# Optimization experiments

Hardware: AMD Instinct MI355X
Metric: run time of the kernel (lower is better)

Reference implementation:

```python
import jax, jax.numpy as jnp
from jax import lax
import numpy as np

B, T, H, K = 32, 512, 2048, 128


def setup_inputs() -> dict:
    key = jax.random.key(0)
    k1, k2, k3, k4, k5, k6, k7 = jax.random.split(key, 7)
    hiddens = jax.random.normal(k1, (B, T, H), dtype=jnp.float32)
    mask = jnp.ones((B, T), dtype=jnp.int32)  # mask[:,0] must be on (torchcrf)
    labels = jax.random.randint(k2, (B, T), 0, K)
    W = jax.random.normal(k3, (H, K), dtype=jnp.float32) * 0.02
    b = jnp.zeros((K,), dtype=jnp.float32)
    # torchcrf inits transitions uniform(-0.1, 0.1)
    start_transitions = jax.random.uniform(k4, (K,), minval=-0.1, maxval=0.1)
    end_transitions = jax.random.uniform(k5, (K,), minval=-0.1, maxval=0.1)
    transitions = jax.random.uniform(k6, (K, K), minval=-0.1, maxval=0.1)
    return {"hiddens": hiddens, "mask": mask, "labels": labels, "W": W, "b": b,
            "start_transitions": start_transitions, "end_transitions": end_transitions,
            "transitions": transitions}


def _crf_log_likelihood(emissions, tags, mask, start_t, end_t, trans):
    # emissions: [B,T,K], tags/mask: [B,T]
    Bn, Tn, Kn = emissions.shape
    maskf = mask.astype(emissions.dtype)
    # ---- numerator: score of the gold path ----
    score = start_t[tags[:, 0]] + emissions[jnp.arange(Bn), 0, tags[:, 0]]
    prev, cur = tags[:, :-1], tags[:, 1:]
    emit_cur = jnp.take_along_axis(emissions[:, 1:], cur[..., None], axis=-1)[..., 0]
    score = score + jnp.sum((trans[prev, cur] + emit_cur) * maskf[:, 1:], axis=1)
    last_idx = mask.sum(axis=1).astype(jnp.int32) - 1
    last_tags = jnp.take_along_axis(tags, last_idx[:, None], axis=1)[:, 0]
    score = score + end_t[last_tags]
    # ---- denominator: log partition via stable logsumexp scan ----
    def step(alpha, inp):
        emit_t, m_t = inp  # [B,K], [B]
        nxt = jax.nn.logsumexp(alpha[:, :, None] + trans[None] + emit_t[:, None, :], axis=1)
        alpha = jnp.where(m_t[:, None] > 0, nxt, alpha)
        return alpha, None
    alpha0 = start_t[None, :] + emissions[:, 0]
    emits = jnp.swapaxes(emissions[:, 1:], 0, 1)  # [T-1,B,K]
    ms = jnp.swapaxes(mask[:, 1:], 0, 1)          # [T-1,B]
    alpha, _ = lax.scan(step, alpha0, (emits, ms))
    logZ = jax.nn.logsumexp(alpha + end_t[None, :], axis=1)
    return score - logZ


def _viterbi_decode(emissions, mask, start_t, end_t, trans):
    Bn, Tn, Kn = emissions.shape
    tag_ids = jnp.arange(Kn, dtype=jnp.int32)
    def step(score, inp):
        emit_t, m_t = inp
        cand = score[:, :, None] + trans[None]          # [B,K,K] prev->cur
        bp = jnp.argmax(cand, axis=1).astype(jnp.int32)  # [B,K]
        best = jnp.max(cand, axis=1) + emit_t
        on = m_t[:, None] > 0
        new_score = jnp.where(on, best, score)
        bp = jnp.where(on, bp, tag_ids[None, :])  # identity for padded steps
        return new_score, bp
    score0 = start_t[None, :] + emissions[:, 0]
    emits = jnp.swapaxes(emissions[:, 1:], 0, 1)
    ms = jnp.swapaxes(mask[:, 1:], 0, 1)
    score, history = lax.scan(step, score0, (emits, ms))  # history: [T-1,B,K]
    last_tag = jnp.argmax(score + end_t[None, :], axis=1).astype(jnp.int32)  # [B]
    def back(tag, bp_t):
        tag = jnp.take_along_axis(bp_t, tag[:, None], axis=1)[:, 0]
        return tag, tag
    _, tags_prev = lax.scan(back, last_tag, history, reverse=True)  # [T-1,B]
    tags = jnp.concatenate([tags_prev, last_tag[None, :]], axis=0)  # [T,B]
    return jnp.swapaxes(tags, 0, 1)  # [B,T]


def reference(hiddens, mask, labels, W, b, start_transitions, end_transitions, transitions):
    logits = jnp.einsum('bth,hk->btk', hiddens, W) + b  # emission projection
    decode = _viterbi_decode(logits, mask, start_transitions, end_transitions, transitions)
    llh = _crf_log_likelihood(logits, labels, mask, start_transitions, end_transitions, transitions)
    loss = -jnp.mean(llh)  # -1 * crf(..., reduction='mean')
    return (decode, loss)
```

## Files before the change

kernel.cpp:

```cpp
#include <hip/hip_runtime.h>
#include <hip/hip_bf16.h>
#include <math.h>

#define BB 32
#define TT 512
#define HH 2048
#define KK 128
#define CH 8
#define NC 32
#define NCV 64

#define WS_LOGITS 0
#define WS_SHIST  8388608u
#define WS_BP     16777216u

__device__ __forceinline__ float quad_add(float x) {
    int a = __builtin_amdgcn_update_dpp(0, __float_as_int(x), 0xB1, 0xF, 0xF, true);
    x += __int_as_float(a);
    int b = __builtin_amdgcn_update_dpp(0, __float_as_int(x), 0x4E, 0xF, 0xF, true);
    x += __int_as_float(b);
    return x;
}
__device__ __forceinline__ float quad_max(float x) {
    int a = __builtin_amdgcn_update_dpp(0, __float_as_int(x), 0xB1, 0xF, 0xF, true);
    x = fmaxf(x, __int_as_float(a));
    int b = __builtin_amdgcn_update_dpp(0, __float_as_int(x), 0x4E, 0xF, 0xF, true);
    x = fmaxf(x, __int_as_float(b));
    return x;
}

__device__ __forceinline__ void step_barrier() {
    __builtin_amdgcn_sched_barrier(0);
    asm volatile("s_waitcnt lgkmcnt(0)" ::: "memory");
    __builtin_amdgcn_sched_barrier(0);
    __builtin_amdgcn_s_barrier();
    __builtin_amdgcn_sched_barrier(0);
}

__global__ __launch_bounds__(512) void gemm_k(const float* __restrict__ hid,
                                              const float* __restrict__ Wm,
                                              const float* __restrict__ bias,
                                              float* __restrict__ logits,
                                              float* __restrict__ loss_slot) {
    __shared__ union {
        struct { float As[4][16][72]; float Bs[4][16][132]; } s;
        float4 red[16][128];
    } sm;
    const int tid = threadIdx.x, bid = blockIdx.x;
    if (bid == 0 && tid == 0) loss_slot[0] = 0.0f;
    const int g = tid >> 7, lt = tid & 127;
    const int rowBase = bid * 64;
    const int rowg = lt >> 4, colg = lt & 15;
    const int arow = lt >> 1, ahq = lt & 1;

    float acc[8][8];
#pragma unroll
    for (int i = 0; i < 8; i++)
#pragma unroll
        for (int j = 0; j < 8; j++) acc[i][j] = 0.0f;

    const float* hA = hid + (size_t)(rowBase + arow) * HH + g * 512 + ahq * 8;

    float4 a0, a1, bv[4];
    {
        const int h0 = g * 512;
        a0 = *(const float4*)(hA);
        a1 = *(const float4*)(hA + 4);
#pragma unroll
        for (int r = 0; r < 4; ++r) {
            int idx = r * 128 + lt;
            bv[r] = *(const float4*)(Wm + (size_t)(h0 + (idx >> 5)) * KK + (idx & 31) * 4);
        }
    }

    for (int it = 0; it < 32; ++it) {
        __syncthreads();
        const int hb = ahq * 8;
        sm.s.As[g][hb + 0][arow] = a0.x;
        sm.s.As[g][hb + 1][arow] = a0.y;
        sm.s.As[g][hb + 2][arow] = a0.z;
        sm.s.As[g][hb + 3][arow] = a0.w;
        sm.s.As[g][hb + 4][arow] = a1.x;
        sm.s.As[g][hb + 5][arow] = a1.y;
        sm.s.As[g][hb + 6][arow] = a1.z;
        sm.s.As[g][hb + 7][arow] = a1.w;
#pragma unroll
        for (int r = 0; r < 4; ++r) {
            int idx = r * 128 + lt;
            *(float4*)&sm.s.Bs[g][idx >> 5][(idx & 31) * 4] = bv[r];
        }
        __syncthreads();
        if (it + 1 < 32) {
            const int h0 = g * 512 + (it + 1) * 16;
            a0 = *(const float4*)(hA + (it + 1) * 16);
            a1 = *(const float4*)(hA + (it + 1) * 16 + 4);
#pragma unroll
            for (int r = 0; r < 4; ++r) {
                int idx = r * 128 + lt;
                bv[r] = *(const float4*)(Wm + (size_t)(h0 + (idx >> 5)) * KK + (idx & 31) * 4);
            }
        }
#pragma unroll
        for (int h = 0; h < 16; ++h) {
            float4 aL = *(const float4*)&sm.s.As[g][h][rowg * 8];
            float4 aH = *(const float4*)&sm.s.As[g][h][rowg * 8 + 4];
            float4 b0 = *(const float4*)&sm.s.Bs[g][h][colg * 4];
            float4 b1 = *(const float4*)&sm.s.Bs[g][h][64 + colg * 4];
            float ar[8] = {aL.x, aL.y, aL.z, aL.w, aH.x, aH.y, aH.z, aH.w};
            float br[8] = {b0.x, b0.y, b0.z, b0.w, b1.x, b1.y, b1.z, b1.w};
#pragma unroll
            for (int i = 0; i < 8; i++)
#pragma unroll
                for (int j = 0; j < 8; j++) acc[i][j] = fmaf(ar[i], br[j], acc[i][j]);
        }
    }
    __syncthreads();
    for (int gp = 1; gp <= 3; ++gp) {
        if (g == gp) {
#pragma unroll
            for (int i = 0; i < 8; ++i) {
                sm.red[i * 2][lt] = make_float4(acc[i][0], acc[i][1], acc[i][2], acc[i][3]);
                sm.red[i * 2 + 1][lt] = make_float4(acc[i][4], acc[i][5], acc[i][6], acc[i][7]);
            }
        }
        __syncthreads();
        if (g == 0) {
#pragma unroll
            for (int i = 0; i < 8; ++i) {
                float4 r0 = sm.red[i * 2][lt];
                float4 r1 = sm.red[i * 2 + 1][lt];
                acc[i][0] += r0.x; acc[i][1] += r0.y; acc[i][2] += r0.z; acc[i][3] += r0.w;
                acc[i][4] += r1.x; acc[i][5] += r1.y; acc[i][6] += r1.z; acc[i][7] += r1.w;
            }
        }
        __syncthreads();
    }
    if (g == 0) {
        float4 bb0 = *(const float4*)(bias + colg * 4);
        float4 bb1 = *(const float4*)(bias + 64 + colg * 4);
#pragma unroll
        for (int i = 0; i < 8; ++i) {
            int row = rowBase + rowg * 8 + i;
            *(float4*)(logits + (size_t)row * KK + colg * 4) =
                make_float4(acc[i][0] + bb0.x, acc[i][1] + bb0.y, acc[i][2] + bb0.z, acc[i][3] + bb0.w);
            *(float4*)(logits + (size_t)row * KK + 64 + colg * 4) =
                make_float4(acc[i][4] + bb1.x, acc[i][5] + bb1.y, acc[i][6] + bb1.z, acc[i][7] + bb1.w);
        }
    }
}

struct SMemB {
    float ubuf[2][144];
    float red[4];
};

__global__ __launch_bounds__(256, 1) void scan_k(const float* __restrict__ logits,
                                                 const int* __restrict__ mask,
                                                 const int* __restrict__ labels,
                                                 const float* __restrict__ startT,
                                                 const float* __restrict__ endT,
                                                 const float* __restrict__ trans,
                                                 float* __restrict__ shist,
                                                 float* __restrict__ out) {
    __shared__ SMemB sm;
    const int tid = threadIdx.x;
    const int bid = blockIdx.x;
    const float L2E = 1.4426950408889634f;
    const int s = tid & 3;
    const int jb = tid >> 2;
    const int j0 = jb * 2;
    const int padw = j0 + 4 * (j0 >> 5);
    const int lane = tid & 63;

    if (bid < BB) {
        const int b = bid;
        const float* lrow = logits + (size_t)b * TT * KK;
        unsigned long long mb[8];
#pragma unroll
        for (int c = 0; c < 8; ++c) mb[c] = __ballot(mask[b * TT + c * 64 + lane] != 0);
        float V0[32], V1[32];
#pragma unroll
        for (int k = 0; k < 32; k++) {
            V0[k] = exp2f(trans[(s * 32 + k) * KK + j0] * L2E);
            V1[k] = exp2f(trans[(s * 32 + k) * KK + j0 + 1] * L2E);
        }
        float a0_ = (startT[j0] + lrow[j0]) * L2E;
        float a1_ = (startT[j0 + 1] + lrow[j0 + 1]) * L2E;
        float OFF = (startT[0] + lrow[0]) * L2E;
        float S0_ = exp2f(a0_ - OFF);
        float S1_ = exp2f(a1_ - OFF);
        if (s == 0) {
            sm.ubuf[0][padw] = S0_;
            sm.ubuf[0][padw + 1] = S1_;
        }
        float2 emc[CH], emn[CH];
#pragma unroll
        for (int d = 0; d < CH; ++d) emc[d] = *(const float2*)(lrow + (size_t)d * KK + j0);
        __syncthreads();
        int cur = 0;
        for (int c = 0; c < NC; ++c) {
#pragma unroll
            for (int r = 0; r < CH; ++r) {
                const int t = c * CH + r;
                if (r == 0 && c + 1 < NC) {
#pragma unroll
                    for (int d = 0; d < CH; ++d)
                        emn[d] = *(const float2*)(lrow + (size_t)((c + 1) * CH + d) * KK + j0);
                }
                if (t > 0 && ((mb[t >> 6] >> (t & 63)) & 1ull)) {
                    const float* ub = &sm.ubuf[cur][s * 36];
                    float u00 = sm.ubuf[cur][0];
                    float uu[32];
#pragma unroll
                    for (int cc = 0; cc < 8; ++cc) {
                        float4 v = *(const float4*)(ub + cc * 4);
                        uu[cc * 4] = v.x; uu[cc * 4 + 1] = v.y; uu[cc * 4 + 2] = v.z; uu[cc * 4 + 3] = v.w;
                    }
                    float2 em = emc[r];
                    float p0e = 0.f, p0o = 0.f, p1e = 0.f, p1o = 0.f;
#pragma unroll
                    for (int k = 0; k < 32; k += 2) {
                        p0e = fmaf(uu[k], V0[k], p0e);
                        p1e = fmaf(uu[k], V1[k], p1e);
                        p0o = fmaf(uu[k + 1], V0[k + 1], p0o);
                        p1o = fmaf(uu[k + 1], V1[k + 1], p1o);
                    }
                    float w0 = quad_add(p0e + p0o);
                    float w1 = quad_add(p1e + p1o);
                    float rinv = __builtin_amdgcn_rcpf(u00);
                    OFF += log2f(u00);
                    S0_ = w0 * (exp2f(em.x * L2E) * rinv);
                    S1_ = w1 * (exp2f(em.y * L2E) * rinv);
                    if (s == 0) {
                        sm.ubuf[cur ^ 1][padw] = S0_;
                        sm.ubuf[cur ^ 1][padw + 1] = S1_;
                    }
                    cur ^= 1;
                }
                step_barrier();
            }
#pragma unroll
            for (int d = 0; d < CH; ++d) emc[d] = emn[d];
        }
        if (s == 0) {
            out[b * TT + j0] = S0_;
            out[b * TT + j0 + 1] = S1_;
        }
        if (tid == 0) out[b * TT + 384] = OFF;

        float part = 0.0f;
        for (int tt = tid; tt < TT; tt += 256) {
            if (tt == 0) {
                int l0 = labels[b * TT];
                part += startT[l0] + lrow[l0];
            } else if (mask[b * TT + tt]) {
                int lc = labels[b * TT + tt];
                int lp = labels[b * TT + tt - 1];
                part += trans[lp * KK + lc] + lrow[(size_t)tt * KK + lc];
            }
        }
#pragma unroll
        for (int d = 1; d < 64; d <<= 1) part += __shfl_xor(part, d, 64);
        int wid = tid >> 6;
        if (lane == 0) sm.red[wid] = part;
        __syncthreads();
        if (tid == 0) {
            int total = 0;
#pragma unroll
            for (int c = 0; c < 8; ++c) total += __popcll(mb[c]);
            float score = sm.red[0] + sm.red[1] + sm.red[2] + sm.red[3];
            score += endT[labels[b * TT + total - 1]];
            out[b * TT + 386] = score;
        }
    } else if (bid < 2 * BB) {
        const int b = bid - BB;
        const float* lrow = logits + (size_t)b * TT * KK;
        unsigned long long mb[4];
#pragma unroll
        for (int c = 0; c < 4; ++c) mb[c] = __ballot(mask[b * TT + 256 + c * 64 + lane] != 0);
        float V0[32], V1[32];
#pragma unroll
        for (int k = 0; k < 32; k++) {
            V0[k] = exp2f(trans[j0 * KK + s * 32 + k] * L2E);
            V1[k] = exp2f(trans[(j0 + 1) * KK + s * 32 + k] * L2E);
        }
        float OFF = endT[0] * L2E;
        float S0_ = exp2f(endT[j0] * L2E - OFF);
        float S1_ = exp2f(endT[j0 + 1] * L2E - OFF);
        {
            float2 e511 = *(const float2*)(lrow + (size_t)511 * KK + j0);
            if (s == 0) {
                sm.ubuf[0][padw] = exp2f(e511.x * L2E) * S0_;
                sm.ubuf[0][padw + 1] = exp2f(e511.y * L2E) * S1_;
            }
        }
        float2 emc[CH], emn[CH];
#pragma unroll
        for (int d = 0; d < CH; ++d) emc[d] = *(const float2*)(lrow + (size_t)(510 - d) * KK + j0);
        __syncthreads();
        int cur = 0;
        for (int c = 0; c < NC; ++c) {
#pragma unroll
            for (int r = 0; r < CH; ++r) {
                const int t = 511 - (c * CH + r);
                if (r == 0 && c + 1 < NC) {
#pragma unroll
                    for (int d = 0; d < CH; ++d)
                        emn[d] = *(const float2*)(lrow + (size_t)(510 - (c + 1) * CH - d) * KK + j0);
                }
                if ((mb[(t - 256) >> 6] >> ((t - 256) & 63)) & 1ull) {
                    const float* ub = &sm.ubuf[cur][s * 36];
                    float u00 = sm.ubuf[cur][0];
                    float uu[32];
#pragma unroll
                    for (int cc = 0; cc < 8; ++cc) {
                        float4 v = *(const float4*)(ub + cc * 4);
                        uu[cc * 4] = v.x; uu[cc * 4 + 1] = v.y; uu[cc * 4 + 2] = v.z; uu[cc * 4 + 3] = v.w;
                    }
                    float p0e = 0.f, p0o = 0.f, p1e = 0.f, p1o = 0.f;
#pragma unroll
                    for (int k = 0; k < 32; k += 2) {
                        p0e = fmaf(uu[k], V0[k], p0e);
                        p1e = fmaf(uu[k], V1[k], p1e);
                        p0o = fmaf(uu[k + 1], V0[k + 1], p0o);
                        p1o = fmaf(uu[k + 1], V1[k + 1], p1o);
                    }
                    float w0 = quad_add(p0e + p0o);
                    float w1 = quad_add(p1e + p1o);
                    float rinv = __builtin_amdgcn_rcpf(u00);
                    OFF += log2f(u00);
                    S0_ = w0 * rinv;
                    S1_ = w1 * rinv;
                }
                float2 em = emc[r];
                if (s == 0) {
                    sm.ubuf[cur ^ 1][padw] = exp2f(em.x * L2E) * S0_;
                    sm.ubuf[cur ^ 1][padw + 1] = exp2f(em.y * L2E) * S1_;
                }
                cur ^= 1;
                step_barrier();
            }
#pragma unroll
            for (int d = 0; d < CH; ++d) emc[d] = emn[d];
        }
        if (s == 0) {
            out[b * TT + 128 + j0] = S0_;
            out[b * TT + 128 + j0 + 1] = S1_;
        }
        if (tid == 0) out[b * TT + 385] = OFF;
    } else {
        const int b = bid - 2 * BB;
        const float* lrow = logits + (size_t)b * TT * KK;
        float* hist = shist + (size_t)b * TT * KK;
        unsigned long long mb[8];
#pragma unroll
        for (int c = 0; c < 8; ++c) mb[c] = __ballot(mask[b * TT + c * 64 + lane] != 0);
        float T0[32], T1[32];
#pragma unroll
        for (int k = 0; k < 32; k++) {
            T0[k] = trans[(s * 32 + k) * KK + j0];
            T1[k] = trans[(s * 32 + k) * KK + j0 + 1];
        }
        float s0_ = startT[j0] + lrow[j0];
        float s1_ = startT[j0 + 1] + lrow[j0 + 1];
        if (s == 0) {
            sm.ubuf[0][padw] = s0_;
            sm.ubuf[0][padw + 1] = s1_;
        } else if (s == 1) {
            *(float2*)(hist + j0) = make_float2(s0_, s1_);
        }
        float2 emc[CH], emn[CH], hb[CH];
#pragma unroll
        for (int d = 0; d < CH; ++d) emc[d] = *(const float2*)(lrow + (size_t)d * KK + j0);
        __syncthreads();
        int cur = 0;
        for (int c = 0; c < NCV; ++c) {
#pragma unroll
            for (int r = 0; r < CH; ++r) {
                const int t = c * CH + r;
                if (r == 0 && c + 1 < NCV) {
#pragma unroll
                    for (int d = 0; d < CH; ++d)
                        emn[d] = *(const float2*)(lrow + (size_t)((c + 1) * CH + d) * KK + j0);
                }
                if (t > 0 && ((mb[t >> 6] >> (t & 63)) & 1ull)) {
                    const float* ub = &sm.ubuf[cur][s * 36];
                    float uu[32];
#pragma unroll
                    for (int cc = 0; cc < 8; ++cc) {
                        float4 v = *(const float4*)(ub + cc * 4);
                        uu[cc * 4] = v.x; uu[cc * 4 + 1] = v.y; uu[cc * 4 + 2] = v.z; uu[cc * 4 + 3] = v.w;
                    }
                    float2 em = emc[r];
                    float m0a = -3.0e38f, m0b = -3.0e38f, m1a = -3.0e38f, m1b = -3.0e38f;
#pragma unroll
                    for (int k = 0; k < 32; k += 4) {
                        m0a = fmaxf(m0a, fmaxf(uu[k] + T0[k], uu[k + 1] + T0[k + 1]));
                        m0b = fmaxf(m0b, fmaxf(uu[k + 2] + T0[k + 2], uu[k + 3] + T0[k + 3]));
                        m1a = fmaxf(m1a, fmaxf(uu[k] + T1[k], uu[k + 1] + T1[k + 1]));
                        m1b = fmaxf(m1b, fmaxf(uu[k + 2] + T1[k + 2], uu[k + 3] + T1[k + 3]));
                    }
                    float m0 = quad_max(fmaxf(m0a, m0b));
                    float m1 = quad_max(fmaxf(m1a, m1b));
                    s0_ = m0 + em.x;
                    s1_ = m1 + em.y;
                    if (s == 0) {
                        sm.ubuf[cur ^ 1][padw] = s0_;
                        sm.ubuf[cur ^ 1][padw + 1] = s1_;
                    }
                    cur ^= 1;
                }
                hb[r] = make_float2(s0_, s1_);
                step_barrier();
            }
            if (s == 1) {
#pragma unroll
                for (int r = 0; r < CH; ++r)
                    *(float2*)(hist + (size_t)(c * CH + r) * KK + j0) = hb[r];
            }
#pragma unroll
            for (int d = 0; d < CH; ++d) emc[d] = emn[d];
        }
    }
}

__global__ __launch_bounds__(256) void bp_k(const float* __restrict__ shist,
                                            const float* __restrict__ trans,
                                            const int* __restrict__ mask,
                                            unsigned char* __restrict__ bp) {
    const int t = blockIdx.x + 1;
    const int tid = threadIdx.x;
    const int j = tid & 127, bg = tid >> 7;
    __shared__ float sc[BB][KK];
#pragma unroll
    for (int r = 0; r < 4; ++r) {
        int f = tid + r * 256;
        int bb2 = f >> 5, c4 = (f & 31) * 4;
        *(float4*)&sc[bb2][c4] = *(const float4*)&shist[(size_t)bb2 * TT * KK + (size_t)(t - 1) * KK + c4];
    }
    __syncthreads();
    float m[16];
    int idx[16];
#pragma unroll
    for (int c = 0; c < 16; c++) { m[c] = -3.0e38f; idx[c] = 0; }
    for (int i4 = 0; i4 < 32; ++i4) {
        const int ib = i4 * 4;
        float tr0 = trans[(ib + 0) * KK + j];
        float tr1 = trans[(ib + 1) * KK + j];
        float tr2 = trans[(ib + 2) * KK + j];
        float tr3 = trans[(ib + 3) * KK + j];
#pragma unroll
        for (int c = 0; c < 16; c++) {
            float4 s4 = *(const float4*)&sc[bg + 2 * c][ib];
            float c0 = s4.x + tr0, c1 = s4.y + tr1, c2 = s4.z + tr2, c3 = s4.w + tr3;
            if (c0 > m[c]) { m[c] = c0; idx[c] = ib; }
            if (c1 > m[c]) { m[c] = c1; idx[c] = ib + 1; }
            if (c2 > m[c]) { m[c] = c2; idx[c] = ib + 2; }
            if (c3 > m[c]) { m[c] = c3; idx[c] = ib + 3; }
        }
    }
#pragma unroll
    for (int c = 0; c < 16; c++) {
        int bb2 = bg + 2 * c;
        int v = idx[c];
        if (mask[bb2 * TT + t] == 0) v = j;
        bp[(size_t)bb2 * TT * KK + (size_t)t * KK + j] = (unsigned char)v;
    }
}

__global__ __launch_bounds__(512) void bt_k(const float* __restrict__ shist,
                                            const float* __restrict__ endT,
                                            const unsigned char* __restrict__ bp,
                                            float* __restrict__ out) {
    const int b = blockIdx.x;
    const int tid = threadIdx.x;
    const int lane = tid & 63, w = tid >> 6;
    __shared__ float cb[128];
    __shared__ float pb[128];
    __shared__ int tagbuf[512];
    __shared__ int handoff;
    if (tid < 128) {
        cb[tid] = shist[(size_t)b * TT * KK + (size_t)(TT - 1) * KK + tid] + endT[tid];
        pb[tid] = out[b * TT + tid] * out[b * TT + 128 + tid];
    }
    float offA = out[b * TT + 384];
    float offB = out[b * TT + 385];
    float score = out[b * TT + 386];
    unsigned int reg[64];
    const unsigned char* bpb = bp + (size_t)b * TT * KK;
#pragma unroll
    for (int r = 0; r < 64; r++) {
        int t_row = w * 64 + 1 + r;
        unsigned int v = 0;
        if (t_row < TT) v = *(const unsigned short*)(bpb + (size_t)t_row * KK + lane * 2);
        reg[r] = v;
    }
    __syncthreads();
    if (tid == 0) {
        float mm = cb[0];
        int bi = 0;
        for (int i = 1; i < 128; i++)
            if (cb[i] > mm) { mm = cb[i]; bi = i; }
        tagbuf[TT - 1] = bi;
        handoff = bi;
        float sum = 0.0f;
        for (int i = 0; i < 128; i++) sum += pb[i];
        float logZ = (offA + offB + log2f(sum)) * 0.6931471805599453f;
        float llh = score - logZ;
        atomicAdd(out + BB * TT, -llh * (1.0f / 32.0f));
    }
    __syncthreads();
    for (int ph = 7; ph >= 0; --ph) {
        if (w == ph) {
            int tag = handoff;
#pragma unroll
            for (int r = 63; r >= 0; --r) {
                int t_row = ph * 64 + 1 + r;
                if (t_row < TT) {
                    unsigned int vv = (unsigned int)__shfl((int)reg[r], tag >> 1, 64);
                    tag = (int)((vv >> ((tag & 1) * 8)) & 0xffu);
                    if (lane == 0) tagbuf[t_row - 1] = tag;
                }
            }
            if (lane == 0) handoff = tag;
        }
        __syncthreads();
    }
    out[b * TT + tid] = (float)tagbuf[tid];
}

extern "C" void kernel_launch(void* const* d_in, const int* in_sizes, int n_in,
                              void* d_out, int out_size, void* d_ws, size_t ws_size,
                              hipStream_t stream) {
    const float* hid = (const float*)d_in[0];
    const int* mask = (const int*)d_in[1];
    const int* labels = (const int*)d_in[2];
    const float* Wm = (const float*)d_in[3];
    const float* bias = (const float*)d_in[4];
    const float* startT = (const float*)d_in[5];
    const float* endT = (const float*)d_in[6];
    const float* trans = (const float*)d_in[7];
    float* out = (float*)d_out;
    char* ws = (char*)d_ws;

    float* logits = (float*)(ws + WS_LOGITS);
    float* shist = (float*)(ws + WS_SHIST);
    unsigned char* bp = (unsigned char*)(ws + WS_BP);

    gemm_k<<<256, 512, 0, stream>>>(hid, Wm, bias, logits, out + BB * TT);
    scan_k<<<96, 256, 0, stream>>>(logits, mask, labels, startT, endT, trans, shist, out);
    bp_k<<<TT - 1, 256, 0, stream>>>(shist, trans, mask, bp);
    bt_k<<<BB, 512, 0, stream>>>(shist, endT, bp, out);
}
```

Measured before the change: 623.6 us.

## Merge forward/backward CRF scans and Viterbi pairs into 512-thread blocks

The forward and backward partition-function scans for one batch now run as two 256-thread halves of a single 512-thread block, each with its own shared buffer. Viterbi scans are likewise packed two batches per block, halving the grid from 96 to 48 blocks. The intent is to use fewer CUs and cut launch and scheduling overhead. The cost is that every per-step barrier now synchronises 8 waves instead of 4, which could lengthen the serial critical path.

```diff
diff --git a/kernel.cpp b/kernel.cpp
--- a/kernel.cpp
+++ b/kernel.cpp
@@ -150,11 +150,11 @@
 }
 
 struct SMemB {
-    float ubuf[2][144];
-    float red[4];
+    float ubuf[2][2][144];
+    float red[8];
 };
 
-__global__ __launch_bounds__(256, 1) void scan_k(const float* __restrict__ logits,
+__global__ __launch_bounds__(512, 1) void scan_k(const float* __restrict__ logits,
                                                  const int* __restrict__ mask,
                                                  const int* __restrict__ labels,
                                                  const float* __restrict__ startT,
@@ -166,190 +166,197 @@
     const int tid = threadIdx.x;
     const int bid = blockIdx.x;
     const float L2E = 1.4426950408889634f;
-    const int s = tid & 3;
-    const int jb = tid >> 2;
+    const int half = tid >> 8;
+    const int htid = tid & 255;
+    const int s = htid & 3;
+    const int jb = htid >> 2;
     const int j0 = jb * 2;
     const int padw = j0 + 4 * (j0 >> 5);
-    const int lane = tid & 63;
+    const int lane = htid & 63;
+    float (*ub2)[144] = sm.ubuf[half];
 
     if (bid < BB) {
         const int b = bid;
         const float* lrow = logits + (size_t)b * TT * KK;
-        unsigned long long mb[8];
-#pragma unroll
-        for (int c = 0; c < 8; ++c) mb[c] = __ballot(mask[b * TT + c * 64 + lane] != 0);
-        float V0[32], V1[32];
-#pragma unroll
-        for (int k = 0; k < 32; k++) {
-            V0[k] = exp2f(trans[(s * 32 + k) * KK + j0] * L2E);
-            V1[k] = exp2f(trans[(s * 32 + k) * KK + j0 + 1] * L2E);
-        }
-        float a0_ = (startT[j0] + lrow[j0]) * L2E;
-        float a1_ = (startT[j0 + 1] + lrow[j0 + 1]) * L2E;
-        float OFF = (startT[0] + lrow[0]) * L2E;
-        float S0_ = exp2f(a0_ - OFF);
-        float S1_ = exp2f(a1_ - OFF);
-        if (s == 0) {
-            sm.ubuf[0][padw] = S0_;
-            sm.ubuf[0][padw + 1] = S1_;
-        }
-        float2 emc[CH], emn[CH];
-#pragma unroll
-        for (int d = 0; d < CH; ++d) emc[d] = *(const float2*)(lrow + (size_t)d * KK + j0);
-        __syncthreads();
-        int cur = 0;
-        for (int c = 0; c < NC; ++c) {
-#pragma unroll
-            for (int r = 0; r < CH; ++r) {
-                const int t = c * CH + r;
-                if (r == 0 && c + 1 < NC) {
-#pragma unroll
-                    for (int d = 0; d < CH; ++d)
-                        emn[d] = *(const float2*)(lrow + (size_t)((c + 1) * CH + d) * KK + j0);
-                }
-                if (t > 0 && ((mb[t >> 6] >> (t & 63)) & 1ull)) {
-                    const float* ub = &sm.ubuf[cur][s * 36];
-                    float u00 = sm.ubuf[cur][0];
-                    float uu[32];
-#pragma unroll
-                    for (int cc = 0; cc < 8; ++cc) {
-                        float4 v = *(const float4*)(ub + cc * 4);
-                        uu[cc * 4] = v.x; uu[cc * 4 + 1] = v.y; uu[cc * 4 + 2] = v.z; uu[cc * 4 + 3] = v.w;
+        if (half == 0) {
+            unsigned long long mb[8];
+#pragma unroll
+            for (int c = 0; c < 8; ++c) mb[c] = __ballot(mask[b * TT + c * 64 + lane] != 0);
+            float V0[32], V1[32];
+#pragma unroll
+            for (int k = 0; k < 32; k++) {
+                V0[k] = exp2f(trans[(s * 32 + k) * KK + j0] * L2E);
+                V1[k] = exp2f(trans[(s * 32 + k) * KK + j0 + 1] * L2E);
+            }
+            float a0_ = (startT[j0] + lrow[j0]) * L2E;
+            float a1_ = (startT[j0 + 1] + lrow[j0 + 1]) * L2E;
+            float OFF = (startT[0] + lrow[0]) * L2E;
+            float S0_ = exp2f(a0_ - OFF);
+            float S1_ = exp2f(a1_ - OFF);
+            if (s == 0) {
+                ub2[0][padw] = S0_;
+                ub2[0][padw + 1] = S1_;
+            }
+            float2 emc[CH], emn[CH];
+#pragma unroll
+            for (int d = 0; d < CH; ++d) emc[d] = *(const float2*)(lrow + (size_t)d * KK + j0);
+            __syncthreads();
+            int cur = 0;
+            for (int c = 0; c < NC; ++c) {
+#pragma unroll
+                for (int r = 0; r < CH; ++r) {
+                    const int t = c * CH + r;
+                    if (r == 0 && c + 1 < NC) {
+#pragma unroll
+                        for (int d = 0; d < CH; ++d)
+                            emn[d] = *(const float2*)(lrow + (size_t)((c + 1) * CH + d) * KK + j0);
+                    }
+                    if (t > 0 && ((mb[t >> 6] >> (t & 63)) & 1ull)) {
+                        const float* ub = &ub2[cur][s * 36];
+                        float u00 = ub2[cur][0];
+                        float uu[32];
+#pragma unroll
+                        for (int cc = 0; cc < 8; ++cc) {
+                            float4 v = *(const float4*)(ub + cc * 4);
+                            uu[cc * 4] = v.x; uu[cc * 4 + 1] = v.y; uu[cc * 4 + 2] = v.z; uu[cc * 4 + 3] = v.w;
+                        }
+                        float2 em = emc[r];
+                        float p0e = 0.f, p0o = 0.f, p1e = 0.f, p1o = 0.f;
+#pragma unroll
+                        for (int k = 0; k < 32; k += 2) {
+                            p0e = fmaf(uu[k], V0[k], p0e);
+                            p1e = fmaf(uu[k], V1[k], p1e);
+                            p0o = fmaf(uu[k + 1], V0[k + 1], p0o);
+                            p1o = fmaf(uu[k + 1], V1[k + 1], p1o);
+                        }
+                        float w0 = quad_add(p0e + p0o);
+                        float w1 = quad_add(p1e + p1o);
+                        float rinv = __builtin_amdgcn_rcpf(u00);
+                        OFF += log2f(u00);
+                        S0_ = w0 * (exp2f(em.x * L2E) * rinv);
+                        S1_ = w1 * (exp2f(em.y * L2E) * rinv);
+                        if (s == 0) {
+                            ub2[cur ^ 1][padw] = S0_;
+                            ub2[cur ^ 1][padw + 1] = S1_;
+                        }
+                        cur ^= 1;
+                    }
+                    step_barrier();
+                }
+#pragma unroll
+                for (int d = 0; d < CH; ++d) emc[d] = emn[d];
+            }
+            if (s == 0) {
+                out[b * TT + j0] = S0_;
+                out[b * TT + j0 + 1] = S1_;
+            }
+            if (htid == 0) out[b * TT + 384] = OFF;
+
+            float part = 0.0f;
+            for (int tt = htid; tt < TT; tt += 256) {
+                if (tt == 0) {
+                    int l0 = labels[b * TT];
+                    part += startT[l0] + lrow[l0];
+                } else if (mask[b * TT + tt]) {
+                    int lc = labels[b * TT + tt];
+                    int lp = labels[b * TT + tt - 1];
+                    part += trans[lp * KK + lc] + lrow[(size_t)tt * KK + lc];
+                }
+            }
+#pragma unroll
+            for (int d = 1; d < 64; d <<= 1) part += __shfl_xor(part, d, 64);
+            int wid = htid >> 6;
+            if (lane == 0) sm.red[wid] = part;
+            if (htid == 0) {
+                int total = 0;
+#pragma unroll
+                for (int c = 0; c < 8; ++c) total += __popcll(mb[c]);
+                sm.red[4] = (float)total;
+            }
+        } else {
+            unsigned long long mb[4];
+#pragma unroll
+            for (int c = 0; c < 4; ++c) mb[c] = __ballot(mask[b * TT + 256 + c * 64 + lane] != 0);
+            float V0[32], V1[32];
+#pragma unroll
+            for (int k = 0; k < 32; k++) {
+                V0[k] = exp2f(trans[j0 * KK + s * 32 + k] * L2E);
+                V1[k] = exp2f(trans[(j0 + 1) * KK + s * 32 + k] * L2E);
+            }
+            float OFF = endT[0] * L2E;
+            float S0_ = exp2f(endT[j0] * L2E - OFF);
+            float S1_ = exp2f(endT[j0 + 1] * L2E - OFF);
+            {
+                float2 e511 = *(const float2*)(lrow + (size_t)511 * KK + j0);
+                if (s == 0) {
+                    ub2[0][padw] = exp2f(e511.x * L2E) * S0_;
+                    ub2[0][padw + 1] = exp2f(e511.y * L2E) * S1_;
+                }
+            }
+            float2 emc[CH], emn[CH];
+#pragma unroll
+            for (int d = 0; d < CH; ++d) emc[d] = *(const float2*)(lrow + (size_t)(510 - d) * KK + j0);
+            __syncthreads();
+            int cur = 0;
+            for (int c = 0; c < NC; ++c) {
+#pragma unroll
+                for (int r = 0; r < CH; ++r) {
+                    const int t = 511 - (c * CH + r);
+                    if (r == 0 && c + 1 < NC) {
+#pragma unroll
+                        for (int d = 0; d < CH; ++d)
+                            emn[d] = *(const float2*)(lrow + (size_t)(510 - (c + 1) * CH - d) * KK + j0);
+                    }
+                    if ((mb[(t - 256) >> 6] >> ((t - 256) & 63)) & 1ull) {
+                        const float* ub = &ub2[cur][s * 36];
+                        float u00 = ub2[cur][0];
+                        float uu[32];
+#pragma unroll
+                        for (int cc = 0; cc < 8; ++cc) {
+                            float4 v = *(const float4*)(ub + cc * 4);
+                            uu[cc * 4] = v.x; uu[cc * 4 + 1] = v.y; uu[cc * 4 + 2] = v.z; uu[cc * 4 + 3] = v.w;
+                        }
+                        float p0e = 0.f, p0o = 0.f, p1e = 0.f, p1o = 0.f;
+#pragma unroll
+                        for (int k = 0; k < 32; k += 2) {
+                            p0e = fmaf(uu[k], V0[k], p0e);
+                            p1e = fmaf(uu[k], V1[k], p1e);
+                            p0o = fmaf(uu[k + 1], V0[k + 1], p0o);
+                            p1o = fmaf(uu[k + 1], V1[k + 1], p1o);
+                        }
+                        float w0 = quad_add(p0e + p0o);
+                        float w1 = quad_add(p1e + p1o);
+                        float rinv = __builtin_amdgcn_rcpf(u00);
+                        OFF += log2f(u00);
+                        S0_ = w0 * rinv;
+                        S1_ = w1 * rinv;
                     }
                     float2 em = emc[r];
-                    float p0e = 0.f, p0o = 0.f, p1e = 0.f, p1o = 0.f;
-#pragma unroll
-                    for (int k = 0; k < 32; k += 2) {
-                        p0e = fmaf(uu[k], V0[k], p0e);
-                        p1e = fmaf(uu[k], V1[k], p1e);
-                        p0o = fmaf(uu[k + 1], V0[k + 1], p0o);
-                        p1o = fmaf(uu[k + 1], V1[k + 1], p1o);
-                    }
-                    float w0 = quad_add(p0e + p0o);
-                    float w1 = quad_add(p1e + p1o);
-                    float rinv = __builtin_amdgcn_rcpf(u00);
-                    OFF += log2f(u00);
-                    S0_ = w0 * (exp2f(em.x * L2E) * rinv);
-                    S1_ = w1 * (exp2f(em.y * L2E) * rinv);
                     if (s == 0) {
-                        sm.ubuf[cur ^ 1][padw] = S0_;
-                        sm.ubuf[cur ^ 1][padw + 1] = S1_;
+                        ub2[cur ^ 1][padw] = exp2f(em.x * L2E) * S0_;
+                        ub2[cur ^ 1][padw + 1] = exp2f(em.y * L2E) * S1_;
                     }
                     cur ^= 1;
-                }
-                step_barrier();
-            }
-#pragma unroll
-            for (int d = 0; d < CH; ++d) emc[d] = emn[d];
-        }
-        if (s == 0) {
-            out[b * TT + j0] = S0_;
-            out[b * TT + j0 + 1] = S1_;
-        }
-        if (tid == 0) out[b * TT + 384] = OFF;
-
-        float part = 0.0f;
-        for (int tt = tid; tt < TT; tt += 256) {
-            if (tt == 0) {
-                int l0 = labels[b * TT];
-                part += startT[l0] + lrow[l0];
-            } else if (mask[b * TT + tt]) {
-                int lc = labels[b * TT + tt];
-                int lp = labels[b * TT + tt - 1];
-                part += trans[lp * KK + lc] + lrow[(size_t)tt * KK + lc];
-            }
-        }
-#pragma unroll
-        for (int d = 1; d < 64; d <<= 1) part += __shfl_xor(part, d, 64);
-        int wid = tid >> 6;
-        if (lane == 0) sm.red[wid] = part;
-        __syncthreads();
-        if (tid == 0) {
-            int total = 0;
-#pragma unroll
-            for (int c = 0; c < 8; ++c) total += __popcll(mb[c]);
+                    step_barrier();
+                }
+#pragma unroll
+                for (int d = 0; d < CH; ++d) emc[d] = emn[d];
+            }
+            if (s == 0) {
+                out[b * TT + 128 + j0] = S0_;
+                out[b * TT + 128 + j0 + 1] = S1_;
+            }
+            if (htid == 0) out[b * TT + 385] = OFF;
+        }
+        __syncthreads();
+        if (half == 0 && htid == 0) {
+            int total = (int)sm.red[4];
             float score = sm.red[0] + sm.red[1] + sm.red[2] + sm.red[3];
             score += endT[labels[b * TT + total - 1]];
             out[b * TT + 386] = score;
         }
-    } else if (bid < 2 * BB) {
-        const int b = bid - BB;
-        const float* lrow = logits + (size_t)b * TT * KK;
-        unsigned long long mb[4];
-#pragma unroll
-        for (int c = 0; c < 4; ++c) mb[c] = __ballot(mask[b * TT + 256 + c * 64 + lane] != 0);
-        float V0[32], V1[32];
-#pragma unroll
-        for (int k = 0; k < 32; k++) {
-            V0[k] = exp2f(trans[j0 * KK + s * 32 + k] * L2E);
-            V1[k] = exp2f(trans[(j0 + 1) * KK + s * 32 + k] * L2E);
-        }
-        float OFF = endT[0] * L2E;
-        float S0_ = exp2f(endT[j0] * L2E - OFF);
-        float S1_ = exp2f(endT[j0 + 1] * L2E - OFF);
-        {
-            float2 e511 = *(const float2*)(lrow + (size_t)511 * KK + j0);
-            if (s == 0) {
-                sm.ubuf[0][padw] = exp2f(e511.x * L2E) * S0_;
-                sm.ubuf[0][padw + 1] = exp2f(e511.y * L2E) * S1_;
-            }
-        }
-        float2 emc[CH], emn[CH];
-#pragma unroll
-        for (int d = 0; d < CH; ++d) emc[d] = *(const float2*)(lrow + (size_t)(510 - d) * KK + j0);
-        __syncthreads();
-        int cur = 0;
-        for (int c = 0; c < NC; ++c) {
-#pragma unroll
-            for (int r = 0; r < CH; ++r) {
-                const int t = 511 - (c * CH + r);
-                if (r == 0 && c + 1 < NC) {
-#pragma unroll
-                    for (int d = 0; d < CH; ++d)
-                        emn[d] = *(const float2*)(lrow + (size_t)(510 - (c + 1) * CH - d) * KK + j0);
-                }
-                if ((mb[(t - 256) >> 6] >> ((t - 256) & 63)) & 1ull) {
-                    const float* ub = &sm.ubuf[cur][s * 36];
-                    float u00 = sm.ubuf[cur][0];
-                    float uu[32];
-#pragma unroll
-                    for (int cc = 0; cc < 8; ++cc) {
-                        float4 v = *(const float4*)(ub + cc * 4);
-                        uu[cc * 4] = v.x; uu[cc * 4 + 1] = v.y; uu[cc * 4 + 2] = v.z; uu[cc * 4 + 3] = v.w;
-                    }
-                    float p0e = 0.f, p0o = 0.f, p1e = 0.f, p1o = 0.f;
-#pragma unroll
-                    for (int k = 0; k < 32; k += 2) {
-                        p0e = fmaf(uu[k], V0[k], p0e);
-                        p1e = fmaf(uu[k], V1[k], p1e);
-                        p0o = fmaf(uu[k + 1], V0[k + 1], p0o);
-                        p1o = fmaf(uu[k + 1], V1[k + 1], p1o);
-                    }
-                    float w0 = quad_add(p0e + p0o);
-                    float w1 = quad_add(p1e + p1o);
-                    float rinv = __builtin_amdgcn_rcpf(u00);
-                    OFF += log2f(u00);
-                    S0_ = w0 * rinv;
-                    S1_ = w1 * rinv;
-                }
-                float2 em = emc[r];
-                if (s == 0) {
-                    sm.ubuf[cur ^ 1][padw] = exp2f(em.x * L2E) * S0_;
-                    sm.ubuf[cur ^ 1][padw + 1] = exp2f(em.y * L2E) * S1_;
-                }
-                cur ^= 1;
-                step_barrier();
-            }
-#pragma unroll
-            for (int d = 0; d < CH; ++d) emc[d] = emn[d];
-        }
-        if (s == 0) {
-            out[b * TT + 128 + j0] = S0_;
-            out[b * TT + 128 + j0 + 1] = S1_;
-        }
-        if (tid == 0) out[b * TT + 385] = OFF;
     } else {
-        const int b = bid - 2 * BB;
+        const int b = (bid - BB) * 2 + half;
         const float* lrow = logits + (size_t)b * TT * KK;
         float* hist = shist + (size_t)b * TT * KK;
         unsigned long long mb[8];
@@ -364,8 +371,8 @@
         float s0_ = startT[j0] + lrow[j0];
         float s1_ = startT[j0 + 1] + lrow[j0 + 1];
         if (s == 0) {
-            sm.ubuf[0][padw] = s0_;
-            sm.ubuf[0][padw + 1] = s1_;
+            ub2[0][padw] = s0_;
+            ub2[0][padw + 1] = s1_;
         } else if (s == 1) {
             *(float2*)(hist + j0) = make_float2(s0_, s1_);
         }
@@ -384,7 +391,7 @@
                         emn[d] = *(const float2*)(lrow + (size_t)((c + 1) * CH + d) * KK + j0);
                 }
                 if (t > 0 && ((mb[t >> 6] >> (t & 63)) & 1ull)) {
-                    const float* ub = &sm.ubuf[cur][s * 36];
+                    const float* ub = &ub2[cur][s * 36];
                     float uu[32];
 #pragma unroll
                     for (int cc = 0; cc < 8; ++cc) {
@@ -405,8 +412,8 @@
                     s0_ = m0 + em.x;
                     s1_ = m1 + em.y;
                     if (s == 0) {
-                        sm.ubuf[cur ^ 1][padw] = s0_;
-                        sm.ubuf[cur ^ 1][padw + 1] = s1_;
+                        ub2[cur ^ 1][padw] = s0_;
+                        ub2[cur ^ 1][padw + 1] = s1_;
                     }
                     cur ^= 1;
                 }
@@ -548,7 +555,7 @@
     unsigned char* bp = (unsigned char*)(ws + WS_BP);
 
     gemm_k<<<256, 512, 0, stream>>>(hid, Wm, bias, logits, out + BB * TT);
-    scan_k<<<96, 256, 0, stream>>>(logits, mask, labels, startT, endT, trans, shist, out);
+    scan_k<<<48, 512, 0, stream>>>(logits, mask, labels, startT, endT, trans, shist, out);
     bp_k<<<TT - 1, 256, 0, stream>>>(shist, trans, mask, bp);
     bt_k<<<BB, 512, 0, stream>>>(shist, endT, bp, out);
 }
```

New measurement: 689.8 us. 1.11x slower.
